# Kernel optimization log

Measured on AMD Instinct MI355X. Metric: run time of the kernel, lower is better.

Reference implementation:

```python
import jax, jax.numpy as jnp
import numpy as np
import math

B, H, S, D = 2, 16, 2048, 64
NEG = -1000000000.0

def setup_inputs() -> dict:
    key = jax.random.key(0)
    kq, kk, kv, km = jax.random.split(key, 4)
    query = jax.random.normal(kq, (B, H, S, D), dtype=jnp.float32)
    k_ = jax.random.normal(kk, (B, H, S, D), dtype=jnp.float32)
    value = jax.random.normal(kv, (B, H, S, D), dtype=jnp.float32)
    mask = jax.random.randint(km, (B, 1, S, S), 0, 2, dtype=jnp.int32)
    return {"query": query, "key": k_, "value": value, "mask": mask}

def reference(query, key, value, mask):
    # scores: [B,H,S,S]
    scale = 1.0 / math.sqrt(query.shape[-1])
    scores = jnp.einsum('bhqd,bhkd->bhqk', query, key) * scale
    scores = jnp.where(mask == 0, NEG, scores)
    # NOTE: original code uses F.softmax(scores, dim=1) -> softmax over the
    # HEAD axis (axis=1) for 4D inputs. Reproduced faithfully.
    p_attn = jax.nn.softmax(scores, axis=1)
    out = jnp.einsum('bhqk,bhkd->bhqd', p_attn, value)
    return (out, p_attn)
```

## Files before the change

### kernel.cpp

```cpp
#include <hip/hip_runtime.h>
#include <hip/hip_bf16.h>
#include <stdint.h>

#define B_ 2
#define H_ 16
#define S_ 2048
#define D_ 64

typedef __attribute__((ext_vector_type(8))) short bf16x8;
typedef __attribute__((ext_vector_type(4))) float f32x4;

__device__ __forceinline__ short f2bf(float x){
  union { float f; uint32_t u; } v; v.f = x;
  uint32_t r = v.u + 0x7FFFu + ((v.u >> 16) & 1u);
  return (short)(r >> 16);
}
__device__ __forceinline__ float bf2f(short s){
  union { uint32_t u; float f; } v; v.u = ((uint32_t)(uint16_t)s) << 16;
  return v.f;
}

__global__ __launch_bounds__(256) void cast_k(const float* __restrict__ K,
                                              short* __restrict__ Khi,
                                              short* __restrict__ Klo){
  size_t idx = ((size_t)blockIdx.x * 256 + threadIdx.x) * 8;
  float4 a = *(const float4*)(K + idx);
  float4 b = *(const float4*)(K + idx + 4);
  float v[8] = {a.x,a.y,a.z,a.w,b.x,b.y,b.z,b.w};
  bf16x8 vh, vl;
  #pragma unroll
  for (int i = 0; i < 8; ++i){
    short hi = f2bf(v[i]);
    vh[i] = hi;
    vl[i] = f2bf(v[i] - bf2f(hi));
  }
  *(bf16x8*)(Khi + idx) = vh;
  *(bf16x8*)(Klo + idx) = vl;
}

__global__ __launch_bounds__(256) void transpose_v(const float* __restrict__ V,
                                                   short* __restrict__ Vt){
  __shared__ float T[64][65];
  int bh = blockIdx.x >> 5;
  int k0 = (blockIdx.x & 31) * 64;
  int t = threadIdx.x;
  {
    int col = (t & 15) * 4;
    #pragma unroll
    for (int i = 0; i < 4; ++i){
      int row = (t >> 4) + i * 16;
      float4 a = *(const float4*)(V + ((size_t)bh * S_ + k0 + row) * D_ + col);
      T[col+0][row] = a.x; T[col+1][row] = a.y; T[col+2][row] = a.z; T[col+3][row] = a.w;
    }
  }
  __syncthreads();
  {
    int d  = t >> 2;
    int kk = (t & 3) * 16;
    bf16x8 o0, o1;
    #pragma unroll
    for (int j = 0; j < 8; ++j){
      o0[j] = f2bf(T[d][kk + j]);
      o1[j] = f2bf(T[d][kk + 8 + j]);
    }
    short* dst = Vt + ((size_t)bh * D_ + d) * S_ + k0 + kk;
    *(bf16x8*)(dst)     = o0;
    *(bf16x8*)(dst + 8) = o1;
  }
}

__global__ __launch_bounds__(1024, 4) void attn_main(
    const float* __restrict__ Q, const short* __restrict__ Khi,
    const short* __restrict__ Klo, const short* __restrict__ Vt,
    const int* __restrict__ mask, float* __restrict__ out,
    float* __restrict__ pout)
{
  __shared__ float sc[2][H_][512];
  __shared__ float zb[2][512];
  __shared__ float cb[2][512];

  const int tid  = threadIdx.x;
  const int h    = tid >> 6;
  const int lane = tid & 63;
  const int g    = lane >> 4;
  const int lr   = lane & 15;

  const int b  = blockIdx.x >> 7;
  const int q0 = (blockIdx.x & 127) << 4;

  const size_t bh = (size_t)b * H_ + h;

  bf16x8 qhi[2], qlo[2];
  {
    const float* qp = Q + (bh * S_ + q0 + lr) * D_ + g * 8;
    #pragma unroll
    for (int c = 0; c < 2; ++c){
      float4 a  = *(const float4*)(qp + c*32);
      float4 d4 = *(const float4*)(qp + c*32 + 4);
      float v[8] = {a.x,a.y,a.z,a.w,d4.x,d4.y,d4.z,d4.w};
      #pragma unroll
      for (int i = 0; i < 8; ++i){
        short hi = f2bf(v[i]);
        qhi[c][i] = hi;
        qlo[c][i] = f2bf(v[i] - bf2f(hi));
      }
    }
  }

  f32x4 o[4];
  #pragma unroll
  for (int j = 0; j < 4; ++j) o[j] = (f32x4){0.f,0.f,0.f,0.f};

  const int swzq = 4 * (lr & 7);

  const short* kbase_hi = Khi + (bh * S_ + lr) * D_ + g * 8;
  const short* kbase_lo = Klo + (bh * S_ + lr) * D_ + g * 8;
  const short* vbase    = Vt  + (bh * D_ + lr) * S_ + g * 8;
  float*       pbase    = pout + (bh * S_ + q0 + lr) * S_ + g * 8;

  for (int it = 0; it < S_/32; ++it){
    const int k0  = it * 32;
    const int buf = it & 1;

    f32x4 s[2];
    #pragma unroll
    for (int t = 0; t < 2; ++t){
      s[t] = (f32x4){0.f,0.f,0.f,0.f};
      #pragma unroll
      for (int c = 0; c < 2; ++c){
        bf16x8 kh = *(const bf16x8*)(kbase_hi + (size_t)(k0 + 16*t) * D_ + c*32);
        bf16x8 kl = *(const bf16x8*)(kbase_lo + (size_t)(k0 + 16*t) * D_ + c*32);
        s[t] = __builtin_amdgcn_mfma_f32_16x16x32_bf16(qhi[c], kh, s[t], 0, 0, 0);
        s[t] = __builtin_amdgcn_mfma_f32_16x16x32_bf16(qlo[c], kh, s[t], 0, 0, 0);
        s[t] = __builtin_amdgcn_mfma_f32_16x16x32_bf16(qhi[c], kl, s[t], 0, 0, 0);
      }
    }
    #pragma unroll
    for (int t = 0; t < 2; ++t){
      #pragma unroll
      for (int r = 0; r < 4; ++r){
        int q = 4*g + r;
        int k = 16*t + lr;
        float e = __expf(s[t][r] * 0.125f);
        sc[buf][h][q*32 + (k ^ (4*(q&7)))] = e;
      }
    }
    __syncthreads();

    if (tid < 512){
      int q = tid >> 5, k = tid & 31;
      int ks = q*32 + (k ^ (4*(q&7)));
      float dsum = 0.f;
      #pragma unroll
      for (int hh = 0; hh < H_; ++hh) dsum += sc[buf][hh][ks];
      int m = __builtin_nontemporal_load(mask + ((size_t)b * S_ + q0 + q) * S_ + k0 + k);
      zb[buf][ks] = m ? (1.0f / dsum) : 0.0f;
      cb[buf][ks] = m ? 0.0f : 0.0625f;
    }
    __syncthreads();

    {
      int b1 = (8*g) ^ swzq;
      int b2 = b1 ^ 4;
      const float* sp = &sc[buf][h][lr*32];
      const float* zp = &zb[buf][lr*32];
      const float* cp = &cb[buf][lr*32];
      float4 e0 = *(const float4*)(sp + b1);
      float4 e1 = *(const float4*)(sp + b2);
      float4 z0 = *(const float4*)(zp + b1);
      float4 z1 = *(const float4*)(zp + b2);
      float4 c0 = *(const float4*)(cp + b1);
      float4 c1 = *(const float4*)(cp + b2);
      float p[8];
      p[0] = e0.x*z0.x + c0.x;  p[1] = e0.y*z0.y + c0.y;
      p[2] = e0.z*z0.z + c0.z;  p[3] = e0.w*z0.w + c0.w;
      p[4] = e1.x*z1.x + c1.x;  p[5] = e1.y*z1.y + c1.y;
      p[6] = e1.z*z1.z + c1.z;  p[7] = e1.w*z1.w + c1.w;

      f32x4 p0 = {p[0],p[1],p[2],p[3]};
      f32x4 p1 = {p[4],p[5],p[6],p[7]};
      __builtin_nontemporal_store(p0, (f32x4*)(pbase + k0));
      __builtin_nontemporal_store(p1, (f32x4*)(pbase + k0 + 4));

      bf16x8 pa;
      #pragma unroll
      for (int i = 0; i < 8; ++i) pa[i] = f2bf(p[i]);

      #pragma unroll
      for (int j = 0; j < 4; ++j){
        bf16x8 vb = *(const bf16x8*)(vbase + (size_t)(16*j) * S_ + k0);
        o[j] = __builtin_amdgcn_mfma_f32_16x16x32_bf16(pa, vb, o[j], 0, 0, 0);
      }
    }
  }

  #pragma unroll
  for (int j = 0; j < 4; ++j){
    #pragma unroll
    for (int r = 0; r < 4; ++r){
      out[(bh * S_ + q0 + 4*g + r) * D_ + 16*j + lr] = o[j][r];
    }
  }
}

extern "C" void kernel_launch(void* const* d_in, const int* in_sizes, int n_in,
                              void* d_out, int out_size, void* d_ws, size_t ws_size,
                              hipStream_t stream){
  const float* Q    = (const float*)d_in[0];
  const float* K    = (const float*)d_in[1];
  const float* V    = (const float*)d_in[2];
  const int*   mask = (const int*)d_in[3];

  const size_t nkv = (size_t)B_ * H_ * S_ * D_;

  short* Khi = (short*)d_ws;
  short* Klo = Khi + nkv;
  short* Vt  = Klo + nkv;

  float* out  = (float*)d_out;
  float* pout = out + nkv;

  cast_k<<<(int)(nkv / (256 * 8)), 256, 0, stream>>>(K, Khi, Klo);
  transpose_v<<<B_ * H_ * (S_ / 64), 256, 0, stream>>>(V, Vt);
  attn_main<<<B_ * (S_ / 16), 1024, 0, stream>>>(Q, Khi, Klo, Vt, mask, out, pout);
}
```

Before: 458.3 us.

## Store exp scores as bf16 in LDS, prefetch mask, raise occupancy bound

The per-head exponentials are now kept in shared memory as bf16 instead of fp32, which halves that buffer, and the launch bound asks for 8 waves per EU instead of 4. The mask value for the next key tile is loaded one iteration early into a register, so its global latency overlaps the QK MFMAs. The stores of the probability output are changed from nontemporal to regular stores. The bf16 rounding of the exponentials lowers the precision of both the head-axis softmax denominators and the stored p_attn, and the tighter register budget could cause spills.

```diff
diff --git a/kernel.cpp b/kernel.cpp
--- a/kernel.cpp
+++ b/kernel.cpp
@@ -9,6 +9,7 @@
 
 typedef __attribute__((ext_vector_type(8))) short bf16x8;
 typedef __attribute__((ext_vector_type(4))) float f32x4;
+typedef __attribute__((ext_vector_type(4))) unsigned short u16x4;
 
 __device__ __forceinline__ short f2bf(float x){
   union { float f; uint32_t u; } v; v.f = x;
@@ -69,13 +70,13 @@
   }
 }
 
-__global__ __launch_bounds__(1024, 4) void attn_main(
+__global__ __launch_bounds__(1024, 8) void attn_main(
     const float* __restrict__ Q, const short* __restrict__ Khi,
     const short* __restrict__ Klo, const short* __restrict__ Vt,
     const int* __restrict__ mask, float* __restrict__ out,
     float* __restrict__ pout)
 {
-  __shared__ float sc[2][H_][512];
+  __shared__ unsigned short sc[2][H_][512];
   __shared__ float zb[2][512];
   __shared__ float cb[2][512];
 
@@ -118,9 +119,16 @@
   const short* vbase    = Vt  + (bh * D_ + lr) * S_ + g * 8;
   float*       pbase    = pout + (bh * S_ + q0 + lr) * S_ + g * 8;
 
+  const int* mp = mask + ((size_t)b * S_ + q0 + ((tid >> 5) & 15)) * S_ + (tid & 31);
+  int mreg = 0;
+  if (tid < 512) mreg = mp[0];
+
   for (int it = 0; it < S_/32; ++it){
     const int k0  = it * 32;
     const int buf = it & 1;
+
+    int mnext = 0;
+    if (tid < 512 && it + 1 < S_/32) mnext = mp[(it + 1) * 32];
 
     f32x4 s[2];
     #pragma unroll
@@ -142,7 +150,7 @@
         int q = 4*g + r;
         int k = 16*t + lr;
         float e = __expf(s[t][r] * 0.125f);
-        sc[buf][h][q*32 + (k ^ (4*(q&7)))] = e;
+        sc[buf][h][q*32 + (k ^ (4*(q&7)))] = (unsigned short)f2bf(e);
       }
     }
     __syncthreads();
@@ -152,35 +160,35 @@
       int ks = q*32 + (k ^ (4*(q&7)));
       float dsum = 0.f;
       #pragma unroll
-      for (int hh = 0; hh < H_; ++hh) dsum += sc[buf][hh][ks];
-      int m = __builtin_nontemporal_load(mask + ((size_t)b * S_ + q0 + q) * S_ + k0 + k);
-      zb[buf][ks] = m ? (1.0f / dsum) : 0.0f;
-      cb[buf][ks] = m ? 0.0f : 0.0625f;
+      for (int hh = 0; hh < H_; ++hh) dsum += bf2f((short)sc[buf][hh][ks]);
+      zb[buf][ks] = mreg ? (1.0f / dsum) : 0.0f;
+      cb[buf][ks] = mreg ? 0.0f : 0.0625f;
     }
     __syncthreads();
 
     {
       int b1 = (8*g) ^ swzq;
       int b2 = b1 ^ 4;
-      const float* sp = &sc[buf][h][lr*32];
+      const unsigned short* sp = &sc[buf][h][lr*32];
       const float* zp = &zb[buf][lr*32];
       const float* cp = &cb[buf][lr*32];
-      float4 e0 = *(const float4*)(sp + b1);
-      float4 e1 = *(const float4*)(sp + b2);
-      float4 z0 = *(const float4*)(zp + b1);
-      float4 z1 = *(const float4*)(zp + b2);
-      float4 c0 = *(const float4*)(cp + b1);
-      float4 c1 = *(const float4*)(cp + b2);
+      u16x4 eh0 = *(const u16x4*)(sp + b1);
+      u16x4 eh1 = *(const u16x4*)(sp + b2);
+      f32x4 z0 = *(const f32x4*)(zp + b1);
+      f32x4 z1 = *(const f32x4*)(zp + b2);
+      f32x4 c0 = *(const f32x4*)(cp + b1);
+      f32x4 c1 = *(const f32x4*)(cp + b2);
       float p[8];
-      p[0] = e0.x*z0.x + c0.x;  p[1] = e0.y*z0.y + c0.y;
-      p[2] = e0.z*z0.z + c0.z;  p[3] = e0.w*z0.w + c0.w;
-      p[4] = e1.x*z1.x + c1.x;  p[5] = e1.y*z1.y + c1.y;
-      p[6] = e1.z*z1.z + c1.z;  p[7] = e1.w*z1.w + c1.w;
+      #pragma unroll
+      for (int j = 0; j < 4; ++j){
+        p[j]     = bf2f((short)eh0[j]) * z0[j] + c0[j];
+        p[4 + j] = bf2f((short)eh1[j]) * z1[j] + c1[j];
+      }
 
       f32x4 p0 = {p[0],p[1],p[2],p[3]};
       f32x4 p1 = {p[4],p[5],p[6],p[7]};
-      __builtin_nontemporal_store(p0, (f32x4*)(pbase + k0));
-      __builtin_nontemporal_store(p1, (f32x4*)(pbase + k0 + 4));
+      *(f32x4*)(pbase + k0)     = p0;
+      *(f32x4*)(pbase + k0 + 4) = p1;
 
       bf16x8 pa;
       #pragma unroll
@@ -192,6 +200,7 @@
         o[j] = __builtin_amdgcn_mfma_f32_16x16x32_bf16(pa, vb, o[j], 0, 0, 0);
       }
     }
+    mreg = mnext;
   }
 
   #pragma unroll
```

New measurement: 807.4 us. 1.76x slower.

## Split head-axis softmax into two passes and drop split-bf16 precision

Applied to the files above, without the earlier changes.

Replaces the single fused kernel, which held all 16 heads per block and synchronized twice per key tile, with two kernels. The first computes the per-(q,k) sum over heads of exp(scores), combines it with the mask into a reciprocal-or-sentinel buffer Z, and writes Z to workspace. The second is a per-head kernel that recomputes scores, normalizes them with Z, writes p_attn, and does P·V through a swizzled LDS tile. It also drops the hi/lo bf16 split for Q and K, using plain bf16 for one MFMA instead of three. In exchange, QK^T is computed twice, a 2048x2048 float Z buffer per batch goes through memory, and score precision is lower.

```diff
diff --git a/kernel.cpp b/kernel.cpp
--- a/kernel.cpp
+++ b/kernel.cpp
@@ -15,27 +15,16 @@
   uint32_t r = v.u + 0x7FFFu + ((v.u >> 16) & 1u);
   return (short)(r >> 16);
 }
-__device__ __forceinline__ float bf2f(short s){
-  union { uint32_t u; float f; } v; v.u = ((uint32_t)(uint16_t)s) << 16;
-  return v.f;
-}
-
-__global__ __launch_bounds__(256) void cast_k(const float* __restrict__ K,
-                                              short* __restrict__ Khi,
-                                              short* __restrict__ Klo){
+
+__global__ __launch_bounds__(256) void cast_bf16(const float* __restrict__ X,
+                                                 short* __restrict__ Y){
   size_t idx = ((size_t)blockIdx.x * 256 + threadIdx.x) * 8;
-  float4 a = *(const float4*)(K + idx);
-  float4 b = *(const float4*)(K + idx + 4);
-  float v[8] = {a.x,a.y,a.z,a.w,b.x,b.y,b.z,b.w};
-  bf16x8 vh, vl;
-  #pragma unroll
-  for (int i = 0; i < 8; ++i){
-    short hi = f2bf(v[i]);
-    vh[i] = hi;
-    vl[i] = f2bf(v[i] - bf2f(hi));
-  }
-  *(bf16x8*)(Khi + idx) = vh;
-  *(bf16x8*)(Klo + idx) = vl;
+  float4 a = *(const float4*)(X + idx);
+  float4 b = *(const float4*)(X + idx + 4);
+  bf16x8 v;
+  v[0]=f2bf(a.x); v[1]=f2bf(a.y); v[2]=f2bf(a.z); v[3]=f2bf(a.w);
+  v[4]=f2bf(b.x); v[5]=f2bf(b.y); v[6]=f2bf(b.z); v[7]=f2bf(b.w);
+  *(bf16x8*)(Y + idx) = v;
 }
 
 __global__ __launch_bounds__(256) void transpose_v(const float* __restrict__ V,
@@ -69,41 +58,81 @@
   }
 }
 
-__global__ __launch_bounds__(1024, 4) void attn_main(
-    const float* __restrict__ Q, const short* __restrict__ Khi,
-    const short* __restrict__ Klo, const short* __restrict__ Vt,
-    const int* __restrict__ mask, float* __restrict__ out,
-    float* __restrict__ pout)
-{
-  __shared__ float sc[2][H_][512];
-  __shared__ float zb[2][512];
-  __shared__ float cb[2][512];
-
-  const int tid  = threadIdx.x;
-  const int h    = tid >> 6;
-  const int lane = tid & 63;
-  const int g    = lane >> 4;
-  const int lr   = lane & 15;
-
-  const int b  = blockIdx.x >> 7;
-  const int q0 = (blockIdx.x & 127) << 4;
-
-  const size_t bh = (size_t)b * H_ + h;
-
-  bf16x8 qhi[2], qlo[2];
-  {
-    const float* qp = Q + (bh * S_ + q0 + lr) * D_ + g * 8;
+__global__ __launch_bounds__(256) void pass1(const float* __restrict__ Q,
+                                             const short* __restrict__ Khi,
+                                             const int* __restrict__ mask,
+                                             float* __restrict__ Z){
+  const int tid = threadIdx.x, w = tid >> 6, lane = tid & 63;
+  const int g = lane >> 4, lr = lane & 15;
+  const int bid = blockIdx.x;
+  const int qg = bid >> 4, b = (bid >> 3) & 1, strip = bid & 7;
+  const int q0 = (qg * 4 + w) * 16;
+  const int ks0 = strip * 256;
+
+  bf16x8 qh[16][2];
+  #pragma unroll
+  for (int h = 0; h < 16; ++h){
+    const float* qp = Q + (((size_t)(b*16 + h)) * S_ + q0 + lr) * D_ + g * 8;
     #pragma unroll
     for (int c = 0; c < 2; ++c){
       float4 a  = *(const float4*)(qp + c*32);
       float4 d4 = *(const float4*)(qp + c*32 + 4);
-      float v[8] = {a.x,a.y,a.z,a.w,d4.x,d4.y,d4.z,d4.w};
-      #pragma unroll
-      for (int i = 0; i < 8; ++i){
-        short hi = f2bf(v[i]);
-        qhi[c][i] = hi;
-        qlo[c][i] = f2bf(v[i] - bf2f(hi));
+      bf16x8 v;
+      v[0]=f2bf(a.x); v[1]=f2bf(a.y); v[2]=f2bf(a.z); v[3]=f2bf(a.w);
+      v[4]=f2bf(d4.x); v[5]=f2bf(d4.y); v[6]=f2bf(d4.z); v[7]=f2bf(d4.w);
+      qh[h][c] = v;
+    }
+  }
+
+  for (int st = 0; st < 16; ++st){
+    const int kk = ks0 + st * 16;
+    f32x4 dsum = (f32x4){0.f,0.f,0.f,0.f};
+    #pragma unroll 4
+    for (int h = 0; h < 16; ++h){
+      f32x4 s = (f32x4){0.f,0.f,0.f,0.f};
+      #pragma unroll
+      for (int c = 0; c < 2; ++c){
+        bf16x8 kh = *(const bf16x8*)(Khi + (((size_t)(b*16 + h)) * S_ + kk + lr) * D_ + c*32 + g*8);
+        s = __builtin_amdgcn_mfma_f32_16x16x32_bf16(qh[h][c], kh, s, 0, 0, 0);
       }
+      #pragma unroll
+      for (int r = 0; r < 4; ++r) dsum[r] += __expf(s[r] * 0.125f);
+    }
+    #pragma unroll
+    for (int r = 0; r < 4; ++r){
+      const size_t qrow = (size_t)b * S_ + q0 + 4*g + r;
+      int m = mask[qrow * S_ + kk + lr];
+      Z[qrow * S_ + kk + lr] = m ? (1.0f / dsum[r]) : -1.0f;
+    }
+  }
+}
+
+__global__ __launch_bounds__(1024) void pass2(const float* __restrict__ Q,
+                                              const short* __restrict__ Khi,
+                                              const short* __restrict__ Vt,
+                                              const float* __restrict__ Z,
+                                              float* __restrict__ out,
+                                              float* __restrict__ pout){
+  __shared__ short pl[16][16][64];
+
+  const int tid = threadIdx.x, w = tid >> 6, lane = tid & 63;
+  const int g = lane >> 4, lr = lane & 15;
+  const int bid = blockIdx.x;
+  const int strip = (bid >> 5) & 7, b = (bid >> 4) & 1, h = bid & 15;
+  const int q0 = strip * 256 + w * 16;
+  const size_t bh = (size_t)b * 16 + h;
+
+  bf16x8 qf[2];
+  {
+    const float* qp = Q + (bh * S_ + q0 + lr) * D_ + g * 8;
+    #pragma unroll
+    for (int c = 0; c < 2; ++c){
+      float4 a  = *(const float4*)(qp + c*32);
+      float4 d4 = *(const float4*)(qp + c*32 + 4);
+      bf16x8 v;
+      v[0]=f2bf(a.x); v[1]=f2bf(a.y); v[2]=f2bf(a.z); v[3]=f2bf(a.w);
+      v[4]=f2bf(d4.x); v[5]=f2bf(d4.y); v[6]=f2bf(d4.z); v[7]=f2bf(d4.w);
+      qf[c] = v;
     }
   }
 
@@ -111,96 +140,70 @@
   #pragma unroll
   for (int j = 0; j < 4; ++j) o[j] = (f32x4){0.f,0.f,0.f,0.f};
 
-  const int swzq = 4 * (lr & 7);
-
-  const short* kbase_hi = Khi + (bh * S_ + lr) * D_ + g * 8;
-  const short* kbase_lo = Klo + (bh * S_ + lr) * D_ + g * 8;
-  const short* vbase    = Vt  + (bh * D_ + lr) * S_ + g * 8;
-  float*       pbase    = pout + (bh * S_ + q0 + lr) * S_ + g * 8;
-
-  for (int it = 0; it < S_/32; ++it){
-    const int k0  = it * 32;
-    const int buf = it & 1;
-
-    f32x4 s[2];
-    #pragma unroll
-    for (int t = 0; t < 2; ++t){
+  const short* kb = Khi + (bh * S_ + lr) * D_ + g * 8;
+  const short* vb = Vt  + (bh * D_ + lr) * S_ + g * 8;
+  const float* zl = Z    + ((size_t)b * S_ + q0 + 4*g) * S_ + lr;
+  float*       pp = pout + (bh * S_ + q0 + 4*g) * S_ + lr;
+  short*       plw = &pl[w][0][0];
+  const int rm = 8 * ((lr ^ (lr >> 3)) & 7);
+
+  for (int it = 0; it < 32; ++it){
+    const int k0 = it * 64;
+
+    f32x4 zv[4];
+    #pragma unroll
+    for (int t = 0; t < 4; ++t)
+      #pragma unroll
+      for (int r = 0; r < 4; ++r)
+        zv[t][r] = zl[(size_t)r * S_ + k0 + 16*t];
+
+    f32x4 s[4];
+    #pragma unroll
+    for (int t = 0; t < 4; ++t){
       s[t] = (f32x4){0.f,0.f,0.f,0.f};
       #pragma unroll
       for (int c = 0; c < 2; ++c){
-        bf16x8 kh = *(const bf16x8*)(kbase_hi + (size_t)(k0 + 16*t) * D_ + c*32);
-        bf16x8 kl = *(const bf16x8*)(kbase_lo + (size_t)(k0 + 16*t) * D_ + c*32);
-        s[t] = __builtin_amdgcn_mfma_f32_16x16x32_bf16(qhi[c], kh, s[t], 0, 0, 0);
-        s[t] = __builtin_amdgcn_mfma_f32_16x16x32_bf16(qlo[c], kh, s[t], 0, 0, 0);
-        s[t] = __builtin_amdgcn_mfma_f32_16x16x32_bf16(qhi[c], kl, s[t], 0, 0, 0);
+        bf16x8 kh = *(const bf16x8*)(kb + (size_t)(k0 + 16*t) * D_ + c*32);
+        s[t] = __builtin_amdgcn_mfma_f32_16x16x32_bf16(qf[c], kh, s[t], 0, 0, 0);
       }
     }
-    #pragma unroll
-    for (int t = 0; t < 2; ++t){
+
+    bf16x8 vr[4][2];
+    #pragma unroll
+    for (int j = 0; j < 4; ++j)
+      #pragma unroll
+      for (int m = 0; m < 2; ++m)
+        vr[j][m] = *(const bf16x8*)(vb + (size_t)(16*j) * S_ + k0 + 32*m);
+
+    #pragma unroll
+    for (int t = 0; t < 4; ++t){
       #pragma unroll
       for (int r = 0; r < 4; ++r){
+        float e = __expf(s[t][r] * 0.125f);
+        float z = zv[t][r];
+        float p = (z < 0.f) ? 0.0625f : e * z;
+        pp[(size_t)r * S_ + k0 + 16*t] = p;
         int q = 4*g + r;
-        int k = 16*t + lr;
-        float e = __expf(s[t][r] * 0.125f);
-        sc[buf][h][q*32 + (k ^ (4*(q&7)))] = e;
+        int ksw = (16*t + lr) ^ (8 * ((q ^ (q >> 3)) & 7));
+        plw[q*64 + ksw] = f2bf(p);
       }
     }
-    __syncthreads();
-
-    if (tid < 512){
-      int q = tid >> 5, k = tid & 31;
-      int ks = q*32 + (k ^ (4*(q&7)));
-      float dsum = 0.f;
-      #pragma unroll
-      for (int hh = 0; hh < H_; ++hh) dsum += sc[buf][hh][ks];
-      int m = __builtin_nontemporal_load(mask + ((size_t)b * S_ + q0 + q) * S_ + k0 + k);
-      zb[buf][ks] = m ? (1.0f / dsum) : 0.0f;
-      cb[buf][ks] = m ? 0.0f : 0.0625f;
-    }
-    __syncthreads();
-
-    {
-      int b1 = (8*g) ^ swzq;
-      int b2 = b1 ^ 4;
-      const float* sp = &sc[buf][h][lr*32];
-      const float* zp = &zb[buf][lr*32];
-      const float* cp = &cb[buf][lr*32];
-      float4 e0 = *(const float4*)(sp + b1);
-      float4 e1 = *(const float4*)(sp + b2);
-      float4 z0 = *(const float4*)(zp + b1);
-      float4 z1 = *(const float4*)(zp + b2);
-      float4 c0 = *(const float4*)(cp + b1);
-      float4 c1 = *(const float4*)(cp + b2);
-      float p[8];
-      p[0] = e0.x*z0.x + c0.x;  p[1] = e0.y*z0.y + c0.y;
-      p[2] = e0.z*z0.z + c0.z;  p[3] = e0.w*z0.w + c0.w;
-      p[4] = e1.x*z1.x + c1.x;  p[5] = e1.y*z1.y + c1.y;
-      p[6] = e1.z*z1.z + c1.z;  p[7] = e1.w*z1.w + c1.w;
-
-      f32x4 p0 = {p[0],p[1],p[2],p[3]};
-      f32x4 p1 = {p[4],p[5],p[6],p[7]};
-      __builtin_nontemporal_store(p0, (f32x4*)(pbase + k0));
-      __builtin_nontemporal_store(p1, (f32x4*)(pbase + k0 + 4));
-
-      bf16x8 pa;
-      #pragma unroll
-      for (int i = 0; i < 8; ++i) pa[i] = f2bf(p[i]);
-
-      #pragma unroll
-      for (int j = 0; j < 4; ++j){
-        bf16x8 vb = *(const bf16x8*)(vbase + (size_t)(16*j) * S_ + k0);
-        o[j] = __builtin_amdgcn_mfma_f32_16x16x32_bf16(pa, vb, o[j], 0, 0, 0);
-      }
+
+    bf16x8 pa0 = *(const bf16x8*)(plw + lr*64 + (( 0 + 8*g) ^ rm));
+    bf16x8 pa1 = *(const bf16x8*)(plw + lr*64 + ((32 + 8*g) ^ rm));
+
+    #pragma unroll
+    for (int j = 0; j < 4; ++j){
+      o[j] = __builtin_amdgcn_mfma_f32_16x16x32_bf16(pa0, vr[j][0], o[j], 0, 0, 0);
+      o[j] = __builtin_amdgcn_mfma_f32_16x16x32_bf16(pa1, vr[j][1], o[j], 0, 0, 0);
     }
   }
 
   #pragma unroll
-  for (int j = 0; j < 4; ++j){
-    #pragma unroll
-    for (int r = 0; r < 4; ++r){
+  for (int j = 0; j < 4; ++j)
+    #pragma unroll
+    for (int r = 0; r < 4; ++r)
       out[(bh * S_ + q0 + 4*g + r) * D_ + 16*j + lr] = o[j][r];
-    }
-  }
 }
 
 extern "C" void kernel_launch(void* const* d_in, const int* in_sizes, int n_in,
@@ -214,13 +217,14 @@
   const size_t nkv = (size_t)B_ * H_ * S_ * D_;
 
   short* Khi = (short*)d_ws;
-  short* Klo = Khi + nkv;
-  short* Vt  = Klo + nkv;
+  short* Vt  = Khi + nkv;
+  float* Zb  = (float*)(Vt + nkv);
 
   float* out  = (float*)d_out;
   float* pout = out + nkv;
 
-  cast_k<<<(int)(nkv / (256 * 8)), 256, 0, stream>>>(K, Khi, Klo);
-  transpose_v<<<B_ * H_ * (S_ / 64), 256, 0, stream>>>(V, Vt);
-  attn_main<<<B_ * (S_ / 16), 1024, 0, stream>>>(Q, Khi, Klo, Vt, mask, out, pout);
-}
+  cast_bf16  <<<(int)(nkv / (256 * 8)), 256, 0, stream>>>(K, Khi);
+  transpose_v<<<B_ * H_ * (S_ / 64),    256, 0, stream>>>(V, Vt);
+  pass1      <<<512,                    256, 0, stream>>>(Q, Khi, mask, Zb);
+  pass2      <<<256,                   1024, 0, stream>>>(Q, Khi, Vt, Zb, out, pout);
+}
```

Result: slower. 603.6 us (+31.7%).
